# Kernel tuning notes

Measured on AMD Instinct MI355X. Metric: run time of the kernel, lower is better.

Reference implementation:

```python
import jax, jax.numpy as jnp
import numpy as np

THR_CONF = 0.5   # threshold_conf
THR_NMS = 0.3    # threshold_nms
K = 1024         # fixed pre-NMS top-k per image (jit-friendly stand-in for boolean filter)
VAR0, VAR1 = 0.1, 0.2  # SSD/RetinaFace decode variances


def setup_inputs() -> dict:
    key = jax.random.key(0)
    k1, k2, k3, k4 = jax.random.split(key, 4)
    B, N = 64, 16800
    p_loc = jax.random.normal(k1, (B, N, 4), jnp.float32)
    p_conf = jax.random.normal(k2, (B, N, 1), jnp.float32)
    p_landms = jax.random.normal(k3, (B, N, 10), jnp.float32)
    # anchor priors in cxcywh, normalized coords
    anchors = jax.random.uniform(k4, (N, 4), jnp.float32, 0.05, 0.6)
    return {"p_loc": p_loc, "p_conf": p_conf, "p_landms": p_landms, "anchors": anchors}


def _decode_boxes(anchors, loc):
    # fix_bbox: cxcy = a_cxcy + loc_xy * var0 * a_wh ; wh = a_wh * exp(loc_wh * var1)
    xy = anchors[..., :2] + loc[..., :2] * VAR0 * anchors[..., 2:]
    wh = anchors[..., 2:] * jnp.exp(loc[..., 2:] * VAR1)
    # xywh2ltrb
    return jnp.concatenate([xy - wh * 0.5, xy + wh * 0.5], axis=-1)  # (B,N,4)


def _decode_kpts(anchors, landms):
    # fix_keypoints: 5 points, each = a_cxcy + d * var0 * a_wh
    B, N, _ = landms.shape
    pts = landms.reshape(B, N, 5, 2)
    kp = anchors[:, None, :2] + pts * VAR0 * anchors[:, None, 2:]
    return kp.reshape(B, N, 10)


def _iou_matrix(b):  # b: (K,4) ltrb -> (K,K)
    area = jnp.maximum(b[:, 2] - b[:, 0], 0.0) * jnp.maximum(b[:, 3] - b[:, 1], 0.0)
    lt = jnp.maximum(b[:, None, :2], b[None, :, :2])
    rb = jnp.minimum(b[:, None, 2:], b[None, :, 2:])
    wh = jnp.maximum(rb - lt, 0.0)
    inter = wh[..., 0] * wh[..., 1]
    return inter / (area[:, None] + area[None, :] - inter + 1e-9)


def _nms_one(boxes, kpts, scores):
    # boxes (N,4), kpts (N,10), scores (N,)
    s = jnp.where(scores >= THR_CONF, scores, -1.0)  # conf mask
    vals, idx = jax.lax.top_k(s, K)                  # sorted candidates (torch nms sorts by score)
    b = boxes[idx]
    kp = kpts[idx]
    iou = _iou_matrix(b)
    ar = jnp.arange(K)

    def body(suppressed, i):
        keep_i = (vals[i] >= THR_CONF) & (~suppressed[i])
        suppressed = suppressed | (keep_i & (iou[i] > THR_NMS) & (ar > i))
        return suppressed, keep_i

    _, keep = jax.lax.scan(body, jnp.zeros(K, dtype=bool), ar)
    m = keep.astype(b.dtype)[:, None]
    # (K,15) = ltrb(4) | keypoints(10) | score(1), zeroed where suppressed/filtered
    return jnp.concatenate([b, kp, vals[:, None]], axis=-1) * m


def reference(p_loc, p_conf, p_landms, anchors):
    scores = jax.nn.sigmoid(p_conf)[..., 0]       # (B,N)
    boxes = _decode_boxes(anchors, p_loc)         # (B,N,4) ltrb
    kpts = _decode_kpts(anchors, p_landms)        # (B,N,10)
    return jax.vmap(_nms_one)(boxes, kpts, scores)  # (B,K,15)
```

## Files before the change

### kernel.cpp

```cpp
#include <hip/hip_runtime.h>
#include <cmath>

#define NB 64
#define NN 16800
#define KK 1024
#define NT 1024
#define CAP 2048
#define RQ 17

typedef unsigned long long ull;

__device__ __forceinline__ unsigned int score_key_f(float cf) {
  if (!(cf >= 0.0f)) return 0u;
  return (__float_as_uint(cf) & 0x7FFFFFFFu) + 1u;
}

__device__ __forceinline__ unsigned int bin_of_key(unsigned int key) {
  float cf = __uint_as_float(key - 1u);
  unsigned int bi = (unsigned int)(int)(cf * 1024.0f);
  return bi > 4095u ? 4095u : bi;
}

__device__ __forceinline__ ull score_key_d(float cf) {
  double s = 1.0 / (1.0 + exp(-(double)cf));
  if (!(s >= 0.5)) return 0ull;
  return ((ull)__double_as_longlong(s) & 0xFFFFFFFFFFFFFull) + 1ull;
}

__device__ __forceinline__ void decode_box_d(const float* lp, const float* ap,
                                             double& X0, double& Y0,
                                             double& X1, double& Y1,
                                             double& AR) {
#pragma clang fp contract(off)
  double l0 = (double)lp[0], l1 = (double)lp[1];
  double l2 = (double)lp[2], l3 = (double)lp[3];
  double a0 = (double)ap[0], a1 = (double)ap[1];
  double a2 = (double)ap[2], a3 = (double)ap[3];
  double xy0 = a0 + (l0 * 0.1) * a2;
  double xy1 = a1 + (l1 * 0.1) * a3;
  double w = a2 * exp(l2 * 0.2);
  double h = a3 * exp(l3 * 0.2);
  X0 = xy0 - w * 0.5; Y0 = xy1 - h * 0.5;
  X1 = xy0 + w * 0.5; Y1 = xy1 + h * 0.5;
  AR = fmax(X1 - X0, 0.0) * fmax(Y1 - Y0, 0.0);
}

__device__ __forceinline__ bool iou_gt_d(double i0, double i1, double i2,
                                         double i3, double ia, double j0,
                                         double j1, double j2, double j3,
                                         double ja) {
#pragma clang fp contract(off)
  double lt0 = fmax(i0, j0), lt1 = fmax(i1, j1);
  double rb0 = fmin(i2, j2), rb1 = fmin(i3, j3);
  double w0 = fmax(rb0 - lt0, 0.0), w1 = fmax(rb1 - lt1, 0.0);
  double inter = w0 * w1;
  double den = ((ia + ja) - inter) + 1e-9;
  return (inter / den) > 0.3;
}

__device__ __forceinline__ float rdlanef(float v, int l) {
  return __uint_as_float(__builtin_amdgcn_readlane(__float_as_uint(v), l));
}

__device__ __forceinline__ ull readlane64(ull v, int l) {
  unsigned int lo = __builtin_amdgcn_readlane((unsigned int)v, l);
  unsigned int hi = __builtin_amdgcn_readlane((unsigned int)(v >> 32), l);
  return ((ull)hi << 32) | (ull)lo;
}

__global__ __launch_bounds__(1024, 1) void sort_kernel(
    const float* __restrict__ p_loc, const float* __restrict__ p_conf,
    const float* __restrict__ anchors, unsigned int* __restrict__ sidx_s,
    float* __restrict__ fbox, float* __restrict__ sval) {
  const int b = blockIdx.x;
  const int tid = threadIdx.x;
  const int lane = tid & 63;
  const int wave = tid >> 6;

  __shared__ unsigned int skey[CAP];
  __shared__ unsigned int sidx[CAP];
  __shared__ unsigned int hist[4096];
  __shared__ unsigned int base[4096];
  __shared__ unsigned int totals[64], chcarry[64];
  __shared__ unsigned int sh_found, sh_binT, sh_cB;
  __shared__ unsigned int scnt, sh_digit, sh_r, sh_c;

  const float* conf = p_conf + (size_t)b * NN;

  unsigned int rkey[RQ];
  #pragma unroll
  for (int q = 0; q < RQ; ++q) {
    const int i = tid + q * NT;
    rkey[q] = (i < NN) ? score_key_f(conf[i]) : 0u;
  }

  for (int i = tid; i < 4096; i += NT) hist[i] = 0u;
  if (tid == 0) sh_found = 0u;
  __syncthreads();
  #pragma unroll
  for (int q = 0; q < RQ; ++q) {
    unsigned int k = rkey[q];
    if (k != 0u) atomicAdd(&hist[bin_of_key(k)], 1u);
  }
  __syncthreads();
  for (int chunk = wave; chunk < 64; chunk += 16) {
    const int bin = chunk * 64 + (63 - lane);
    unsigned int c0 = hist[bin];
    unsigned int x = c0;
    #pragma unroll
    for (int d = 1; d < 64; d <<= 1) {
      unsigned int y = __shfl_up(x, d);
      if (lane >= d) x += y;
    }
    base[bin] = x;
    if (lane == 63) totals[chunk] = x;
  }
  __syncthreads();
  if (wave == 0) {
    const int chunk = 63 - lane;
    unsigned int t0 = totals[chunk];
    unsigned int x = t0;
    #pragma unroll
    for (int d = 1; d < 64; d <<= 1) {
      unsigned int y = __shfl_up(x, d);
      if (lane >= d) x += y;
    }
    chcarry[chunk] = x - t0;
  }
  __syncthreads();
  for (int chunk = wave; chunk < 64; chunk += 16) {
    const int bin = chunk * 64 + (63 - lane);
    unsigned int c0 = hist[bin];
    unsigned int S = chcarry[chunk] + base[bin] - c0;
    base[bin] = S;
    if (S < (unsigned)KK && (unsigned)KK <= S + c0) {
      sh_found = 1u; sh_binT = (unsigned int)bin; sh_cB = c0;
    }
  }
  __syncthreads();
  const bool fastOK = (sh_found != 0u) && (sh_cB <= 64u);
  const unsigned int binT = sh_binT;

  if (fastOK) {
    for (int i = tid; i < KK + 64; i += NT) { skey[i] = 0u; sidx[i] = 0xFFFFFFFFu; }
    __syncthreads();
    #pragma unroll
    for (int q = 0; q < RQ; ++q) {
      const int i = tid + q * NT;
      unsigned int k = rkey[q];
      if (k != 0u) {
        unsigned int bin = bin_of_key(k);
        if (bin >= binT) {
          unsigned int pos = atomicAdd(&base[bin], 1u);
          if (pos < (unsigned)(KK + 64)) { skey[pos] = k; sidx[pos] = (unsigned int)i; }
        }
      }
    }
    __syncthreads();
    for (int bin = (int)binT + tid; bin < 4096; bin += NT) {
      unsigned int cnt = hist[bin];
      if (cnt >= 2u) {
        int hi2 = (int)base[bin];
        int lo2 = hi2 - (int)cnt;
        for (int m2 = lo2 + 1; m2 < hi2; ++m2) {
          unsigned int kx = skey[m2]; unsigned int ix = sidx[m2];
          int n2 = m2;
          while (n2 > lo2) {
            unsigned int kp = skey[n2 - 1]; unsigned int ip = sidx[n2 - 1];
            bool after = (kp < kx) || (kp == kx && ip > ix);
            if (!after) break;
            skey[n2] = kp; sidx[n2] = ip; --n2;
          }
          skey[n2] = kx; sidx[n2] = ix;
        }
      }
    }
    __syncthreads();
  } else {
    unsigned int r = KK;
    unsigned int prefix = 0u, T = 0u;
    for (int pass = 0; pass < 4; ++pass) {
      const int shift = 24 - pass * 8;
      if (tid < 256) hist[tid] = 0u;
      __syncthreads();
      const unsigned int pm = pass ? ~((1u << (shift + 8)) - 1u) : 0u;
      #pragma unroll
      for (int q = 0; q < RQ; ++q) {
        unsigned int k = rkey[q];
        if (k != 0u && (k & pm) == prefix)
          atomicAdd(&hist[(k >> shift) & 255u], 1u);
      }
      __syncthreads();
      if (wave == 0) {
        if (lane == 0) { sh_digit = 0u; sh_r = r; sh_c = 0u; }
        unsigned int carry = 0;
        for (int chunk = 3; chunk >= 0; --chunk) {
          const int bin = chunk * 64 + (63 - lane);
          unsigned int c = hist[bin];
          unsigned int x = c;
          #pragma unroll
          for (int d = 1; d < 64; d <<= 1) {
            unsigned int y = __shfl_up(x, d);
            if (lane >= d) x += y;
          }
          unsigned int excl = x - c;
          unsigned int S = carry + excl;
          bool hit = (S < r) && (r <= S + c);
          ull bal = __ballot(hit ? 1 : 0);
          if (bal != 0ull) {
            int hl = __ffsll((long long)bal) - 1;
            unsigned int Sf = __shfl(S, hl);
            unsigned int bf = __shfl((unsigned int)bin, hl);
            unsigned int cf2 = __shfl(c, hl);
            if (lane == 0) { sh_digit = bf; sh_r = r - Sf; sh_c = cf2; }
            break;
          }
          carry += __shfl(x, 63);
        }
      }
      __syncthreads();
      prefix |= (sh_digit << shift);
      r = sh_r;
      const unsigned int cntge = (KK - r) + sh_c;
      if (cntge <= CAP || pass == 3) { T = prefix; break; }
    }

    if (tid == 0) scnt = 0u;
    for (int i = tid; i < CAP; i += NT) { skey[i] = 0u; sidx[i] = 0xFFFFFFFFu; }
    __syncthreads();
    #pragma unroll
    for (int q = 0; q < RQ; ++q) {
      const int i = tid + q * NT;
      unsigned int k = rkey[q];
      if (k != 0u && k >= T) {
        unsigned int pos = atomicAdd(&scnt, 1u);
        if (pos < CAP) { skey[pos] = k; sidx[pos] = (unsigned int)i; }
      }
    }
    __syncthreads();

    for (unsigned int k2 = 2; k2 <= CAP; k2 <<= 1) {
      for (unsigned int j = k2 >> 1; j > 0; j >>= 1) {
        for (int i = tid; i < CAP; i += NT) {
          int ixj = i ^ (int)j;
          if (ixj > i) {
            bool up = ((i & k2) == 0);
            unsigned int ka = skey[i], kbv = skey[ixj];
            unsigned int ia = sidx[i], ib = sidx[ixj];
            bool a_after_b = (ka < kbv) || (ka == kbv && ia > ib);
            if (a_after_b == up) {
              skey[i] = kbv; skey[ixj] = ka;
              sidx[i] = ib; sidx[ixj] = ia;
            }
          }
        }
        __syncthreads();
      }
    }
  }

  const unsigned int mykey = skey[tid];
  const unsigned int myidx = sidx[tid];
  double X0 = 0.0, Y0 = 0.0, X1 = 0.0, Y1 = 0.0, AR = 0.0;
  float v = -1.0f;
  if (mykey != 0u) {
    decode_box_d(p_loc + ((size_t)b * NN + myidx) * 4,
                 anchors + (size_t)myidx * 4, X0, Y0, X1, Y1, AR);
    double s = 1.0 / (1.0 + exp(-(double)conf[myidx]));
    v = (float)s;
  }
  sidx_s[(size_t)b * KK + tid] = myidx;
  float* fb = fbox + (size_t)b * 5 * KK;
  fb[0 * KK + tid] = (float)X0; fb[1 * KK + tid] = (float)Y0;
  fb[2 * KK + tid] = (float)X1; fb[3 * KK + tid] = (float)Y1;
  fb[4 * KK + tid] = (float)AR;
  sval[(size_t)b * KK + tid] = v;
}

__global__ __launch_bounds__(256) void pair_kernel(
    const float* __restrict__ p_loc, const float* __restrict__ anchors,
    const unsigned int* __restrict__ sidx_s, const float* __restrict__ fbox,
    const float* __restrict__ sval, ull* __restrict__ maskg) {
  const int img = blockIdx.x;
  const int wave = threadIdx.x >> 6;
  const int lane = threadIdx.x & 63;
  const int t = blockIdx.y * 4 + wave;

  int rg = 0, rem = t;
  while (rem >= 16 - rg) { rem -= 16 - rg; ++rg; }
  const int cg = rg + rem;

  const int rgs = __builtin_amdgcn_readfirstlane(rg);

  const float* fb = fbox + (size_t)img * 5 * KK;
  const int irow = rgs * 64 + lane;
  const int jcol = cg * 64 + lane;

  const float* rb0 = fb + 0 * KK + rgs * 64;
  const float* rb1 = fb + 1 * KK + rgs * 64;
  const float* rb2 = fb + 2 * KK + rgs * 64;
  const float* rb3 = fb + 3 * KK + rgs * 64;
  const float* rba = fb + 4 * KK + rgs * 64;

  unsigned int ri = sidx_s[(size_t)img * KK + irow];

  const float cj0 = fb[0 * KK + jcol], cj1 = fb[1 * KK + jcol];
  const float cj2 = fb[2 * KK + jcol], cj3 = fb[3 * KK + jcol];
  const float caj = fb[4 * KK + jcol];
  const unsigned int cidx = sidx_s[(size_t)img * KK + jcol];

  unsigned int wlo = 0u, whi = 0u;

  #pragma unroll 8
  for (int rr = 0; rr < 64; ++rr) {
    const float bi0 = rb0[rr], bi1 = rb1[rr];
    const float bi2 = rb2[rr], bi3 = rb3[rr];
    const float ai = rba[rr];
    float lt0 = fmaxf(bi0, cj0), lt1 = fmaxf(bi1, cj1);
    float q0 = fminf(bi2, cj2), q1 = fminf(bi3, cj3);
    float w0 = fmaxf(q0 - lt0, 0.0f), w1 = fmaxf(q1 - lt1, 0.0f);
    float inter = w0 * w1;
    float den = ((ai + caj) - inter) + 1e-9f;
    float d = inter - 0.3f * den;
    bool bit = d > 0.0f;
    bool unc = fabsf(d) <= den * 1e-3f;
    if (__builtin_expect((bool)__ballot(unc ? 1 : 0), 0)) {
      const unsigned int rbi = __builtin_amdgcn_readlane(ri, rr);
      if (unc) {
        double rX0, rY0, rX1, rY1, rAR, qX0, qY0, qX1, qY1, qAR;
        decode_box_d(p_loc + ((size_t)img * NN + rbi) * 4,
                     anchors + (size_t)rbi * 4, rX0, rY0, rX1, rY1, rAR);
        decode_box_d(p_loc + ((size_t)img * NN + cidx) * 4,
                     anchors + (size_t)cidx * 4, qX0, qY0, qX1, qY1, qAR);
        bit = iou_gt_d(rX0, rY0, rX1, rY1, rAR, qX0, qY0, qX1, qY1, qAR);
      }
    }
    bit = bit && (jcol > rgs * 64 + rr);
    ull m = __ballot(bit ? 1 : 0);
    const bool mine = (lane == rr);
    wlo = mine ? (unsigned int)m : wlo;
    whi = mine ? (unsigned int)(m >> 32) : whi;
  }

  maskg[((size_t)img * KK + (size_t)rgs * 64 + lane) * 16 + cg] =
      ((ull)whi << 32) | (ull)wlo;
}

__global__ __launch_bounds__(1024, 1) void resolve_kernel(
    const float* __restrict__ p_landms, const float* __restrict__ anchors,
    const unsigned int* __restrict__ sidx_s, const float* __restrict__ fbox,
    const float* __restrict__ sval, const ull* __restrict__ maskg,
    float* __restrict__ out) {
  const int img = blockIdx.x, tid = threadIdx.x, lane = tid & 63,
            wave = tid >> 6;
  __shared__ ull buf[2][2048];
  __shared__ float svbuf[KK];
  __shared__ ull keepw[16];
  const ull* mg = maskg + (size_t)img * KK * 16;

  svbuf[tid] = sval[(size_t)img * KK + tid];
  for (int u = tid; u < 2048; u += NT) buf[0][u] = mg[u];
  __syncthreads();

  ull supw = 0ull;
  for (int s = 0; s < 8; ++s) {
    const int cur = s & 1;
    if (wave != 0) {
      if (s + 1 < 8) {
        const ull* src = mg + (size_t)(s + 1) * 2048;
        const int wmin = 2 * (s + 1);
        for (int u = tid - 64; u < 2048; u += NT - 64)
          if ((u & 15) >= wmin) buf[cur ^ 1][u] = src[u];
      }
    } else {
      #pragma unroll
      for (int half = 0; half < 2; ++half) {
        const int g = 2 * s + half;
        const ull vm = __ballot(svbuf[g * 64 + lane] >= 0.0f);
        ull curw = readlane64(supw, g);
        ull km = 0ull;
        #pragma unroll 8
        for (int rr = 0; rr < 64; ++rr) {
          const int rl = half * 64 + rr;
          ull mw = 0ull;
          if (lane < 16 && lane >= g) mw = buf[cur][rl * 16 + lane];
          const bool keep = (((vm >> rr) & 1ull) != 0ull) &&
                            (((curw >> rr) & 1ull) == 0ull);
          if (keep) {
            km |= (1ull << rr);
            supw |= mw;
            curw |= readlane64(mw, g);
          }
        }
        if (lane == 0) keepw[g] = km;
      }
    }
    __syncthreads();
  }

  const bool keep = ((keepw[tid >> 6] >> (tid & 63)) & 1ull) != 0ull;
  float* op = out + ((size_t)img * KK + tid) * 15;
  if (keep) {
    const float* fb = fbox + (size_t)img * 5 * KK;
    op[0] = fb[0 * KK + tid]; op[1] = fb[1 * KK + tid];
    op[2] = fb[2 * KK + tid]; op[3] = fb[3 * KK + tid];
    const unsigned int myidx = sidx_s[(size_t)img * KK + tid];
    const float* pp = p_landms + ((size_t)img * NN + myidx) * 10;
    const float* ap = anchors + (size_t)myidx * 4;
    double a0 = (double)ap[0], a1 = (double)ap[1];
    double a2 = (double)ap[2], a3 = (double)ap[3];
    #pragma unroll
    for (int q = 0; q < 5; ++q) {
      double px = (double)pp[2 * q], py = (double)pp[2 * q + 1];
      op[4 + 2 * q]     = (float)(a0 + (px * 0.1) * a2);
      op[4 + 2 * q + 1] = (float)(a1 + (py * 0.1) * a3);
    }
    op[14] = svbuf[tid];
  } else {
    #pragma unroll
    for (int q = 0; q < 15; ++q) op[q] = 0.0f;
  }
}

__global__ __launch_bounds__(1024, 1) void fallback_kernel(
    const float* __restrict__ p_loc, const float* __restrict__ p_conf,
    const float* __restrict__ p_landms, const float* __restrict__ anchors,
    const ull* __restrict__ gkeys, float* __restrict__ out) {
  const int b = blockIdx.x;
  const int tid = threadIdx.x;
  const int lane = tid & 63;
  const int wave = tid >> 6;

  __shared__ ull skey[CAP];
  __shared__ unsigned int sidx[CAP];
  __shared__ float fb0[KK], fb1[KK], fb2[KK], fb3[KK], farr[KK];
  __shared__ float svalf[KK];
  __shared__ ull chunkmask[32][16];
  __shared__ unsigned int keepm[32];
  __shared__ ull supShared[16];
  __shared__ unsigned int hist[256];
  __shared__ unsigned int scnt, sh_digit, sh_r;

  unsigned long long rkey[RQ];
  if (gkeys != nullptr) {
    const ull* kb = gkeys + (size_t)b * NN;
    #pragma unroll
    for (int q = 0; q < RQ; ++q) {
      const int i = tid + q * NT;
      rkey[q] = (i < NN) ? kb[i] : 0ull;
    }
  } else {
    const float* conf = p_conf + (size_t)b * NN;
    #pragma unroll
    for (int q = 0; q < RQ; ++q) {
      const int i = tid + q * NT;
      rkey[q] = (i < NN) ? score_key_d(conf[i]) : 0ull;
    }
  }

  unsigned int r = KK;
  ull prefix = 0ull;
  for (int pass = 0; pass < 7; ++pass) {
    const int shift = 48 - pass * 8;
    if (tid < 256) hist[tid] = 0u;
    __syncthreads();
    const ull pm = (pass == 0) ? 0ull : ~((1ull << (shift + 8)) - 1ull);
    #pragma unroll
    for (int q = 0; q < RQ; ++q) {
      const int i = tid + q * NT;
      if (i < NN) {
        ull k = rkey[q];
        if (k != 0ull && (k & pm) == prefix)
          atomicAdd(&hist[(unsigned int)(k >> shift) & 255u], 1u);
      }
    }
    __syncthreads();
    if (wave == 0) {
      if (lane == 0) { sh_digit = 0u; sh_r = r; }
      unsigned int carry = 0;
      for (int chunk = 3; chunk >= 0; --chunk) {
        const int bin = chunk * 64 + (63 - lane);
        unsigned int c = hist[bin];
        unsigned int x = c;
        #pragma unroll
        for (int d = 1; d < 64; d <<= 1) {
          unsigned int y = __shfl_up(x, d);
          if (lane >= d) x += y;
        }
        unsigned int excl = x - c;
        unsigned int S = carry + excl;
        bool hit = (S < r) && (r <= S + c);
        ull bal = __ballot(hit ? 1 : 0);
        if (bal != 0ull) {
          int hl = __ffsll((long long)bal) - 1;
          unsigned int Sf = __shfl(S, hl);
          unsigned int bf = __shfl((unsigned int)bin, hl);
          if (lane == 0) { sh_digit = bf; sh_r = r - Sf; }
          break;
        }
        carry += __shfl(x, 63);
      }
    }
    __syncthreads();
    prefix |= ((ull)sh_digit << shift);
    r = sh_r;
    __syncthreads();
  }
  const ull T = prefix;

  if (tid == 0) scnt = 0u;
  for (int i = tid; i < CAP; i += NT) { skey[i] = 0ull; sidx[i] = 0xFFFFFFFFu; }
  __syncthreads();
  #pragma unroll
  for (int q = 0; q < RQ; ++q) {
    const int i = tid + q * NT;
    if (i < NN) {
      ull k = rkey[q];
      if (k != 0ull && k >= T) {
        unsigned int pos = atomicAdd(&scnt, 1u);
        if (pos < CAP) { skey[pos] = k; sidx[pos] = (unsigned int)i; }
      }
    }
  }
  __syncthreads();

  for (unsigned int k2 = 2; k2 <= CAP; k2 <<= 1) {
    for (unsigned int j = k2 >> 1; j > 0; j >>= 1) {
      for (int i = tid; i < CAP; i += NT) {
        int ixj = i ^ (int)j;
        if (ixj > i) {
          bool up = ((i & k2) == 0);
          ull ka = skey[i], kb = skey[ixj];
          unsigned int ia = sidx[i], ib = sidx[ixj];
          bool a_after_b = (ka < kb) || (ka == kb && ia > ib);
          if (a_after_b == up) {
            skey[i] = kb; skey[ixj] = ka;
            sidx[i] = ib; sidx[ixj] = ia;
          }
        }
      }
      __syncthreads();
    }
  }

  const ull mykey = skey[tid];
  const unsigned int myidx = sidx[tid];
  double dX0 = 0.0, dY0 = 0.0, dX1 = 0.0, dY1 = 0.0, dAR = 0.0;
  {
    float v = -1.0f;
    if (mykey != 0ull) {
      decode_box_d(p_loc + ((size_t)b * NN + myidx) * 4,
                   anchors + (size_t)myidx * 4, dX0, dY0, dX1, dY1, dAR);
      double s = __longlong_as_double(
          (long long)(0x3FE0000000000000ull | (mykey - 1ull)));
      v = (float)s;
    }
    fb0[tid] = (float)dX0; fb1[tid] = (float)dY0;
    fb2[tid] = (float)dX1; fb3[tid] = (float)dY1;
    farr[tid] = (float)dAR;
    svalf[tid] = v;
  }
  if (tid < 16) supShared[tid] = 0ull;
  if (tid < 32) keepm[tid] = 0u;
  __syncthreads();

  const float cj0 = fb0[tid], cj1 = fb1[tid], cj2 = fb2[tid], cj3 = fb3[tid];
  const float caj = farr[tid];
  ull supw = 0ull;

  for (int c = 0; c < 32; ++c) {
    for (int rr = 0; rr < 32; ++rr) {
      const int i = c * 32 + rr;
      const bool rowDead =
          (svalf[i] < 0.0f) ||
          (((supShared[i >> 6] >> (i & 63)) & 1ull) != 0ull);
      if (rowDead) continue;
      float bi0 = fb0[i], bi1 = fb1[i], bi2 = fb2[i], bi3 = fb3[i];
      float ai = farr[i];
      float lt0 = fmaxf(bi0, cj0), lt1 = fmaxf(bi1, cj1);
      float q0 = fminf(bi2, cj2), q1 = fminf(bi3, cj3);
      float w0 = fmaxf(q0 - lt0, 0.0f), w1 = fmaxf(q1 - lt1, 0.0f);
      float inter = w0 * w1;
      float den = ((ai + caj) - inter) + 1e-9f;
      float d = inter - 0.3f * den;
      bool bit = d > 0.0f;
      bool unc = fabsf(d) <= den * 1e-3f;
      if (__builtin_expect((bool)__ballot(unc ? 1 : 0), 0)) {
        if (unc) {
          const unsigned int ridx = sidx[i];
          double rX0, rY0, rX1, rY1, rAR;
          decode_box_d(p_loc + ((size_t)b * NN + ridx) * 4,
                       anchors + (size_t)ridx * 4, rX0, rY0, rX1, rY1, rAR);
          bit = iou_gt_d(rX0, rY0, rX1, rY1, rAR, dX0, dY0, dX1, dY1, dAR);
        }
      }
      bit = bit && (tid > i);
      ull m = __ballot(bit ? 1 : 0);
      if (lane == 0) chunkmask[rr][wave] = m;
    }
    __syncthreads();
    if (wave == 0) {
      unsigned int km = 0u;
      for (int rr = 0; rr < 32; ++rr) {
        const int i = c * 32 + rr;
        ull sc = __shfl(supw, i >> 6);
        bool keep = (svalf[i] >= 0.0f) && (((sc >> (i & 63)) & 1ull) == 0ull);
        if (keep) {
          km |= (1u << rr);
          if (lane < 16) supw |= chunkmask[rr][lane];
        }
      }
      if (lane == 0) keepm[c] = km;
      if (lane < 16) supShared[lane] = supw;
    }
    __syncthreads();
  }

  {
    const bool keep = ((keepm[tid >> 5] >> (tid & 31)) & 1u) != 0u;
    float* op = out + ((size_t)b * KK + tid) * 15;
    if (keep) {
      op[0] = fb0[tid]; op[1] = fb1[tid]; op[2] = fb2[tid]; op[3] = fb3[tid];
      const float* pp = p_landms + ((size_t)b * NN + myidx) * 10;
      const float* ap = anchors + (size_t)myidx * 4;
      double a0 = (double)ap[0], a1 = (double)ap[1];
      double a2 = (double)ap[2], a3 = (double)ap[3];
      #pragma unroll
      for (int q = 0; q < 5; ++q) {
        double px = (double)pp[2 * q], py = (double)pp[2 * q + 1];
        op[4 + 2 * q]     = (float)(a0 + (px * 0.1) * a2);
        op[4 + 2 * q + 1] = (float)(a1 + (py * 0.1) * a3);
      }
      op[14] = svalf[tid];
    } else {
      #pragma unroll
      for (int q = 0; q < 15; ++q) op[q] = 0.0f;
    }
  }
}

extern "C" void kernel_launch(void* const* d_in, const int* in_sizes, int n_in,
                              void* d_out, int out_size, void* d_ws, size_t ws_size,
                              hipStream_t stream) {
  const float* p_loc    = (const float*)d_in[0];
  const float* p_conf   = (const float*)d_in[1];
  const float* p_landms = (const float*)d_in[2];
  const float* anchors  = (const float*)d_in[3];
  float* out = (float*)d_out;
  (void)in_sizes; (void)n_in; (void)out_size;

  const size_t off_sidx = 0;
  const size_t off_fbox = off_sidx + (size_t)NB * KK * 4;
  const size_t off_sval = off_fbox + (size_t)NB * 5 * KK * 4;
  const size_t off_mask = off_sval + (size_t)NB * KK * 4;
  const size_t mask_bytes = (size_t)NB * KK * 16 * sizeof(ull);
  const size_t total = off_mask + mask_bytes;

  char* ws = (char*)d_ws;

  if (ws_size >= total) {
    unsigned int* sidx_s = (unsigned int*)(ws + off_sidx);
    float* fbox = (float*)(ws + off_fbox);
    float* sval = (float*)(ws + off_sval);
    ull* maskg = (ull*)(ws + off_mask);

    hipLaunchKernelGGL(sort_kernel, dim3(NB), dim3(NT), 0, stream,
                       p_loc, p_conf, anchors, sidx_s, fbox, sval);
    hipLaunchKernelGGL(pair_kernel, dim3(NB, 34), dim3(256), 0, stream,
                       p_loc, anchors, sidx_s, fbox, sval, maskg);
    hipLaunchKernelGGL(resolve_kernel, dim3(NB), dim3(NT), 0, stream,
                       p_landms, anchors, sidx_s, fbox, sval, maskg, out);
  } else {
    hipLaunchKernelGGL(fallback_kernel, dim3(NB), dim3(NT), 0, stream,
                       p_loc, p_conf, p_landms, anchors, (const ull*)nullptr,
                       out);
  }
}
```

Baseline: 207.5 us.

## Split NMS greedy scan into serial diagonal pass and parallel row-OR reduction

Wave 0's greedy suppression loop now carries only the diagonal 64-bit block serially, each lane holding one row's diagonal word and broadcasting it by readlane. Propagating suppression to the later column words is deferred: after the block's keep mask is known, 64 lanes OR the kept rows' masks in parallel and combine partial results with cross-lane shuffles. This cuts per-iteration LDS loads and divergent branches from the serial critical path. The cost is an extra reduction phase of shuffles per block.

Result: faster. 199.9 us (-3.7%).

```diff
diff --git a/kernel.cpp b/kernel.cpp
--- a/kernel.cpp
+++ b/kernel.cpp
@@ -65,6 +65,18 @@
 __device__ __forceinline__ ull readlane64(ull v, int l) {
   unsigned int lo = __builtin_amdgcn_readlane((unsigned int)v, l);
   unsigned int hi = __builtin_amdgcn_readlane((unsigned int)(v >> 32), l);
+  return ((ull)hi << 32) | (ull)lo;
+}
+
+__device__ __forceinline__ ull shfl64(ull v, int src) {
+  unsigned int lo = (unsigned int)__shfl((int)(unsigned int)v, src);
+  unsigned int hi = (unsigned int)__shfl((int)(unsigned int)(v >> 32), src);
+  return ((ull)hi << 32) | (ull)lo;
+}
+
+__device__ __forceinline__ ull shflxor64(ull v, int m) {
+  unsigned int lo = (unsigned int)__shfl_xor((int)(unsigned int)v, m);
+  unsigned int hi = (unsigned int)__shfl_xor((int)(unsigned int)(v >> 32), m);
   return ((ull)hi << 32) | (ull)lo;
 }
 
@@ -377,22 +389,35 @@
       for (int half = 0; half < 2; ++half) {
         const int g = 2 * s + half;
         const ull vm = __ballot(svbuf[g * 64 + lane] >= 0.0f);
+        const ull diagw = buf[cur][(half * 64 + lane) * 16 + g];
         ull curw = readlane64(supw, g);
         ull km = 0ull;
         #pragma unroll 8
         for (int rr = 0; rr < 64; ++rr) {
-          const int rl = half * 64 + rr;
-          ull mw = 0ull;
-          if (lane < 16 && lane >= g) mw = buf[cur][rl * 16 + lane];
-          const bool keep = (((vm >> rr) & 1ull) != 0ull) &&
-                            (((curw >> rr) & 1ull) == 0ull);
-          if (keep) {
-            km |= (1ull << rr);
-            supw |= mw;
-            curw |= readlane64(mw, g);
+          const ull mw = readlane64(diagw, rr);
+          const ull bitm = 1ull << rr;
+          const ull keepbit = (vm & ~curw) & bitm;
+          km |= keepbit;
+          curw |= (keepbit != 0ull) ? mw : 0ull;
+        }
+        if (lane == 0) keepw[g] = km;
+        if (g < 15) {
+          const int w = lane >> 2, sub = lane & 3;
+          ull acc = 0ull;
+          #pragma unroll
+          for (int t2 = 0; t2 < 16; ++t2) {
+            const int rr = sub * 16 + t2;
+            ull mv = buf[cur][(half * 64 + rr) * 16 + w];
+            const ull kb = (km >> rr) & 1ull;
+            acc |= (kb != 0ull) ? mv : 0ull;
           }
-        }
-        if (lane == 0) keepw[g] = km;
+          if (w < g) acc = 0ull;
+          acc |= shflxor64(acc, 1);
+          acc |= shflxor64(acc, 2);
+          const ull g4 = shfl64(acc, (lane & 15) * 4);
+          if (lane < 16) supw |= g4;
+          if (lane == g) supw = curw;
+        }
       }
     }
     __syncthreads();
```

## Replace pairwise IoU mask kernels with fused on-the-fly greedy NMS

Applied to the files above, without the earlier changes.

Removes the separate pair kernel that built a full 1024x1024 IoU suppression bitmask per image and the resolve kernel that consumed it. A single block-per-image kernel now loads the boxes into shared memory and, for each kept candidate only, computes IoU against all columns. Suppression bits are merged via shared memory with two barriers per kept box. This avoids computing IoU for suppressed rows and the global mask round-trip, at the cost of serialization proportional to the number of kept boxes.

Result: slower. 223.6 us (+7.7%).

```diff
diff --git a/kernel.cpp b/kernel.cpp
--- a/kernel.cpp
+++ b/kernel.cpp
@@ -56,16 +56,6 @@
   double inter = w0 * w1;
   double den = ((ia + ja) - inter) + 1e-9;
   return (inter / den) > 0.3;
-}
-
-__device__ __forceinline__ float rdlanef(float v, int l) {
-  return __uint_as_float(__builtin_amdgcn_readlane(__float_as_uint(v), l));
-}
-
-__device__ __forceinline__ ull readlane64(ull v, int l) {
-  unsigned int lo = __builtin_amdgcn_readlane((unsigned int)v, l);
-  unsigned int hi = __builtin_amdgcn_readlane((unsigned int)(v >> 32), l);
-  return ((ull)hi << 32) | (ull)lo;
 }
 
 __global__ __launch_bounds__(1024, 1) void sort_kernel(
@@ -277,134 +267,86 @@
   sval[(size_t)b * KK + tid] = v;
 }
 
-__global__ __launch_bounds__(256) void pair_kernel(
-    const float* __restrict__ p_loc, const float* __restrict__ anchors,
-    const unsigned int* __restrict__ sidx_s, const float* __restrict__ fbox,
-    const float* __restrict__ sval, ull* __restrict__ maskg) {
-  const int img = blockIdx.x;
-  const int wave = threadIdx.x >> 6;
-  const int lane = threadIdx.x & 63;
-  const int t = blockIdx.y * 4 + wave;
-
-  int rg = 0, rem = t;
-  while (rem >= 16 - rg) { rem -= 16 - rg; ++rg; }
-  const int cg = rg + rem;
-
-  const int rgs = __builtin_amdgcn_readfirstlane(rg);
-
-  const float* fb = fbox + (size_t)img * 5 * KK;
-  const int irow = rgs * 64 + lane;
-  const int jcol = cg * 64 + lane;
-
-  const float* rb0 = fb + 0 * KK + rgs * 64;
-  const float* rb1 = fb + 1 * KK + rgs * 64;
-  const float* rb2 = fb + 2 * KK + rgs * 64;
-  const float* rb3 = fb + 3 * KK + rgs * 64;
-  const float* rba = fb + 4 * KK + rgs * 64;
-
-  unsigned int ri = sidx_s[(size_t)img * KK + irow];
-
-  const float cj0 = fb[0 * KK + jcol], cj1 = fb[1 * KK + jcol];
-  const float cj2 = fb[2 * KK + jcol], cj3 = fb[3 * KK + jcol];
-  const float caj = fb[4 * KK + jcol];
-  const unsigned int cidx = sidx_s[(size_t)img * KK + jcol];
-
-  unsigned int wlo = 0u, whi = 0u;
-
-  #pragma unroll 8
-  for (int rr = 0; rr < 64; ++rr) {
-    const float bi0 = rb0[rr], bi1 = rb1[rr];
-    const float bi2 = rb2[rr], bi3 = rb3[rr];
-    const float ai = rba[rr];
-    float lt0 = fmaxf(bi0, cj0), lt1 = fmaxf(bi1, cj1);
-    float q0 = fminf(bi2, cj2), q1 = fminf(bi3, cj3);
-    float w0 = fmaxf(q0 - lt0, 0.0f), w1 = fmaxf(q1 - lt1, 0.0f);
-    float inter = w0 * w1;
-    float den = ((ai + caj) - inter) + 1e-9f;
-    float d = inter - 0.3f * den;
-    bool bit = d > 0.0f;
-    bool unc = fabsf(d) <= den * 1e-3f;
-    if (__builtin_expect((bool)__ballot(unc ? 1 : 0), 0)) {
-      const unsigned int rbi = __builtin_amdgcn_readlane(ri, rr);
-      if (unc) {
-        double rX0, rY0, rX1, rY1, rAR, qX0, qY0, qX1, qY1, qAR;
-        decode_box_d(p_loc + ((size_t)img * NN + rbi) * 4,
-                     anchors + (size_t)rbi * 4, rX0, rY0, rX1, rY1, rAR);
-        decode_box_d(p_loc + ((size_t)img * NN + cidx) * 4,
-                     anchors + (size_t)cidx * 4, qX0, qY0, qX1, qY1, qAR);
-        bit = iou_gt_d(rX0, rY0, rX1, rY1, rAR, qX0, qY0, qX1, qY1, qAR);
-      }
-    }
-    bit = bit && (jcol > rgs * 64 + rr);
-    ull m = __ballot(bit ? 1 : 0);
-    const bool mine = (lane == rr);
-    wlo = mine ? (unsigned int)m : wlo;
-    whi = mine ? (unsigned int)(m >> 32) : whi;
-  }
-
-  maskg[((size_t)img * KK + (size_t)rgs * 64 + lane) * 16 + cg] =
-      ((ull)whi << 32) | (ull)wlo;
-}
-
-__global__ __launch_bounds__(1024, 1) void resolve_kernel(
-    const float* __restrict__ p_landms, const float* __restrict__ anchors,
-    const unsigned int* __restrict__ sidx_s, const float* __restrict__ fbox,
-    const float* __restrict__ sval, const ull* __restrict__ maskg,
+__global__ __launch_bounds__(1024, 1) void nms_kernel(
+    const float* __restrict__ p_loc, const float* __restrict__ p_landms,
+    const float* __restrict__ anchors, const unsigned int* __restrict__ sidx_s,
+    const float* __restrict__ fbox, const float* __restrict__ sval,
     float* __restrict__ out) {
   const int img = blockIdx.x, tid = threadIdx.x, lane = tid & 63,
             wave = tid >> 6;
-  __shared__ ull buf[2][2048];
+  __shared__ float fb0[KK], fb1[KK], fb2[KK], fb3[KK], farr[KK];
   __shared__ float svbuf[KK];
-  __shared__ ull keepw[16];
-  const ull* mg = maskg + (size_t)img * KK * 16;
-
+  __shared__ unsigned int sxbuf[KK];
+  __shared__ ull sup[16], mword[16], keepw[16], vmw[16];
+
+  const float* fb = fbox + (size_t)img * 5 * KK;
+  fb0[tid] = fb[0 * KK + tid]; fb1[tid] = fb[1 * KK + tid];
+  fb2[tid] = fb[2 * KK + tid]; fb3[tid] = fb[3 * KK + tid];
+  farr[tid] = fb[4 * KK + tid];
   svbuf[tid] = sval[(size_t)img * KK + tid];
-  for (int u = tid; u < 2048; u += NT) buf[0][u] = mg[u];
-  __syncthreads();
-
-  ull supw = 0ull;
-  for (int s = 0; s < 8; ++s) {
-    const int cur = s & 1;
-    if (wave != 0) {
-      if (s + 1 < 8) {
-        const ull* src = mg + (size_t)(s + 1) * 2048;
-        const int wmin = 2 * (s + 1);
-        for (int u = tid - 64; u < 2048; u += NT - 64)
-          if ((u & 15) >= wmin) buf[cur ^ 1][u] = src[u];
-      }
-    } else {
-      #pragma unroll
-      for (int half = 0; half < 2; ++half) {
-        const int g = 2 * s + half;
-        const ull vm = __ballot(svbuf[g * 64 + lane] >= 0.0f);
-        ull curw = readlane64(supw, g);
-        ull km = 0ull;
-        #pragma unroll 8
-        for (int rr = 0; rr < 64; ++rr) {
-          const int rl = half * 64 + rr;
-          ull mw = 0ull;
-          if (lane < 16 && lane >= g) mw = buf[cur][rl * 16 + lane];
-          const bool keep = (((vm >> rr) & 1ull) != 0ull) &&
-                            (((curw >> rr) & 1ull) == 0ull);
-          if (keep) {
-            km |= (1ull << rr);
-            supw |= mw;
-            curw |= readlane64(mw, g);
+  sxbuf[tid] = sidx_s[(size_t)img * KK + tid];
+  if (tid < 16) { sup[tid] = 0ull; keepw[tid] = 0ull; }
+  __syncthreads();
+  {
+    const ull vm = __ballot(svbuf[wave * 64 + lane] >= 0.0f);
+    if (lane == 0) vmw[wave] = vm;
+  }
+  const float cj0 = fb0[tid], cj1 = fb1[tid], cj2 = fb2[tid], cj3 = fb3[tid];
+  const float caj = farr[tid];
+  const unsigned int cidx = sxbuf[tid];
+  __syncthreads();
+
+  for (int g = 0; g < 16; ++g) {
+    ull supg = sup[g];
+    const ull vmg = vmw[g];
+    ull keepg = 0ull;
+    for (int r = 0; r < 64; ++r) {
+      const ull bm = 1ull << r;
+      const bool keep = ((vmg & ~supg) & bm) != 0ull;
+      if (keep) {
+        const int i = g * 64 + r;
+        keepg |= bm;
+        const float bi0 = fb0[i], bi1 = fb1[i];
+        const float bi2 = fb2[i], bi3 = fb3[i];
+        const float ai = farr[i];
+        float lt0 = fmaxf(bi0, cj0), lt1 = fmaxf(bi1, cj1);
+        float q0 = fminf(bi2, cj2), q1 = fminf(bi3, cj3);
+        float w0 = fmaxf(q0 - lt0, 0.0f), w1 = fmaxf(q1 - lt1, 0.0f);
+        float inter = w0 * w1;
+        float den = ((ai + caj) - inter) + 1e-9f;
+        float d = inter - 0.3f * den;
+        bool bit = d > 0.0f;
+        bool unc = fabsf(d) <= den * 1e-3f;
+        if (__builtin_expect((bool)__ballot(unc ? 1 : 0), 0)) {
+          if (unc) {
+            const unsigned int ridx = sxbuf[i];
+            double rX0, rY0, rX1, rY1, rAR, qX0, qY0, qX1, qY1, qAR;
+            decode_box_d(p_loc + ((size_t)img * NN + ridx) * 4,
+                         anchors + (size_t)ridx * 4, rX0, rY0, rX1, rY1, rAR);
+            decode_box_d(p_loc + ((size_t)img * NN + cidx) * 4,
+                         anchors + (size_t)cidx * 4, qX0, qY0, qX1, qY1, qAR);
+            bit = iou_gt_d(rX0, rY0, rX1, rY1, rAR, qX0, qY0, qX1, qY1, qAR);
           }
         }
-        if (lane == 0) keepw[g] = km;
-      }
-    }
-    __syncthreads();
-  }
+        bit = bit && (tid > i);
+        const ull m = __ballot(bit ? 1 : 0);
+        if (lane == 0) mword[wave] = m;
+        __syncthreads();
+        supg |= mword[g];
+        if (tid < 16) sup[tid] |= mword[tid];
+        __syncthreads();
+      }
+    }
+    if (tid == 0) keepw[g] = keepg;
+  }
+  __syncthreads();
 
   const bool keep = ((keepw[tid >> 6] >> (tid & 63)) & 1ull) != 0ull;
   float* op = out + ((size_t)img * KK + tid) * 15;
   if (keep) {
-    const float* fb = fbox + (size_t)img * 5 * KK;
-    op[0] = fb[0 * KK + tid]; op[1] = fb[1 * KK + tid];
-    op[2] = fb[2 * KK + tid]; op[3] = fb[3 * KK + tid];
-    const unsigned int myidx = sidx_s[(size_t)img * KK + tid];
+    op[0] = fb0[tid]; op[1] = fb1[tid];
+    op[2] = fb2[tid]; op[3] = fb3[tid];
+    const unsigned int myidx = sxbuf[tid];
     const float* pp = p_landms + ((size_t)img * NN + myidx) * 10;
     const float* ap = anchors + (size_t)myidx * 4;
     double a0 = (double)ap[0], a1 = (double)ap[1];
@@ -652,9 +594,7 @@
   const size_t off_sidx = 0;
   const size_t off_fbox = off_sidx + (size_t)NB * KK * 4;
   const size_t off_sval = off_fbox + (size_t)NB * 5 * KK * 4;
-  const size_t off_mask = off_sval + (size_t)NB * KK * 4;
-  const size_t mask_bytes = (size_t)NB * KK * 16 * sizeof(ull);
-  const size_t total = off_mask + mask_bytes;
+  const size_t total = off_sval + (size_t)NB * KK * 4;
 
   char* ws = (char*)d_ws;
 
@@ -662,14 +602,11 @@
     unsigned int* sidx_s = (unsigned int*)(ws + off_sidx);
     float* fbox = (float*)(ws + off_fbox);
     float* sval = (float*)(ws + off_sval);
-    ull* maskg = (ull*)(ws + off_mask);
 
     hipLaunchKernelGGL(sort_kernel, dim3(NB), dim3(NT), 0, stream,
                        p_loc, p_conf, anchors, sidx_s, fbox, sval);
-    hipLaunchKernelGGL(pair_kernel, dim3(NB, 34), dim3(256), 0, stream,
-                       p_loc, anchors, sidx_s, fbox, sval, maskg);
-    hipLaunchKernelGGL(resolve_kernel, dim3(NB), dim3(NT), 0, stream,
-                       p_landms, anchors, sidx_s, fbox, sval, maskg, out);
+    hipLaunchKernelGGL(nms_kernel, dim3(NB), dim3(NT), 0, stream,
+                       p_loc, p_landms, anchors, sidx_s, fbox, sval, out);
   } else {
     hipLaunchKernelGGL(fallback_kernel, dim3(NB), dim3(NT), 0, stream,
                        p_loc, p_conf, p_landms, anchors, (const ull*)nullptr,
```
